# Kernel optimization log

Hardware: AMD Instinct MI355X
Metric: run time of the kernel (lower is better)

Reference implementation:

```python
import jax, jax.numpy as jnp
import numpy as np

E = 512      # moe_experts
M = 6        # per-expert dim = moe_dim // 2
H = 6        # moe_heads
D = 1024     # hidden_size
F = E * M    # flatten_shape = 3072

def relu2(x):
    return jnp.square(jax.nn.relu(x))

def setup_inputs() -> dict:
    key = jax.random.key(0)
    ks = jax.random.split(key, 12)
    B, S = 4, 2048
    inp = {
        "x": jax.random.normal(ks[0], (B, S, D), jnp.float32),
        "g1": jax.random.uniform(ks[1], (B, S, H, E), jnp.float32),
        "g2": jax.random.uniform(ks[2], (B, S, H, E), jnp.float32),
        "u1_w": jax.random.normal(ks[3], (F, D), jnp.float32) * 0.02,
        "u1_b": jnp.zeros((F,), jnp.float32),
        "u2_w": jax.random.normal(ks[4], (F, D), jnp.float32) * 0.02,
        "u2_b": jnp.zeros((F,), jnp.float32),
        "v11_w": jax.random.normal(ks[5], (D // 2, F), jnp.float32) * 0.02,
        "v12_w": jax.random.normal(ks[6], (D // 2, F), jnp.float32) * 0.02,
        "v21_w": jax.random.normal(ks[7], (D // 2, F), jnp.float32) * 0.02,
        "v22_w": jax.random.normal(ks[8], (D // 2, F), jnp.float32) * 0.02,
        "b1": jnp.zeros((E, D // 2), jnp.float32),
        "b2": jnp.zeros((E, D // 2), jnp.float32),
    }
    return inp

def reference(x, g1, g2, u1_w, u1_b, u2_w, u2_b, v11_w, v12_w, v21_w, v22_w, b1, b2):
    B, S, _ = x.shape
    # up-proj + relu^2, split into (experts E, per-expert dim M)
    x1 = relu2(x @ u1_w.T + u1_b).reshape(B, S, E, M)   # [B,S,E,M]
    x2 = relu2(x @ u2_w.T + u2_b).reshape(B, S, E, M)
    # gate sums over heads
    gs1 = jnp.einsum('bshi,bsim->bsim', g1, x1)          # sum_h g1 applied to x1
    gs2 = jnp.einsum('bshj,bsjm->bsjm', g2, x2)
    x11 = gs1.reshape(B, S, F) @ v11_w.T                 # [B,S,D/2]
    x22 = gs2.reshape(B, S, F) @ v22_w.T
    # cross terms: contract over h efficiently (avoid E x E materialization)
    t2 = jnp.einsum('bshj,bsjm->bshm', g2, x2)           # [B,S,H,M]
    x12 = jnp.einsum('bshm,bshi->bsim', t2, g1).reshape(B, S, F) @ v12_w.T
    t1 = jnp.einsum('bshi,bsim->bshm', g1, x1)
    x21 = jnp.einsum('bshm,bshj->bsjm', t1, g2).reshape(B, S, F) @ v21_w.T
    # bias terms through gates
    x13 = jnp.einsum('bshi,id->bsd', g1, b1)
    x23 = jnp.einsum('bshj,jd->bsd', g2, b2)
    return jnp.concatenate((x11 + x12 + x13, x21 + x22 + x23), axis=-1)
```

## Files before the change

### kernel.cpp

```cpp
#include <hip/hip_runtime.h>
#include <stdint.h>

typedef unsigned short u16;
typedef unsigned int u32;
typedef __attribute__((ext_vector_type(8))) short bf16x8;
typedef __attribute__((ext_vector_type(4))) float f32x4;

__device__ __forceinline__ float bf2f(u16 u) {
    unsigned v = ((unsigned)u) << 16;
    float f;
    __builtin_memcpy(&f, &v, 4);
    return f;
}
__device__ __forceinline__ u16 f2bf(float f) {
    unsigned x;
    __builtin_memcpy(&x, &f, 4);
    unsigned r = (x + 0x7fffu + ((x >> 16) & 1u)) >> 16;
    return (u16)r;
}

#define GLDS(g, l) __builtin_amdgcn_global_load_lds( \
    (const __attribute__((address_space(1))) void*)(g), \
    (__attribute__((address_space(3))) void*)(l), 16, 0, 0)

#define BARX() do { asm volatile("" ::: "memory"); __builtin_amdgcn_s_barrier(); asm volatile("" ::: "memory"); } while (0)
#define LGKM0() asm volatile("s_waitcnt lgkmcnt(0)" ::: "memory")
#define WAIT_VM4() asm volatile("s_waitcnt vmcnt(4)" ::: "memory")
#define WAIT_VM0() asm volatile("s_waitcnt vmcnt(0)" ::: "memory")

__device__ __forceinline__ void gemm256_core(
    const u16* gA, const u16* gB, size_t ldk, int NT,
    u16* lds, int tid, f32x4 (&acc)[8][4])
{
    const int lane  = tid & 63;
    const int wave  = tid >> 6;
    const int wr    = wave >> 2;
    const int wc    = wave & 3;
    const int mlane = lane & 15;
    const int quad  = lane >> 4;
    const int swz   = mlane & 7;

    u16* A0 = lds;
    u16* B0 = lds + 16384;
    u16* A1 = lds + 32768;
    u16* B1 = lds + 49152;

    #define ST_A(h, t, dst) do { \
        GLDS(gA + (size_t)((h)*128     ) * ldk + (size_t)(t) * 64, (dst) + (h)*8192 + tid*8); \
        GLDS(gA + (size_t)((h)*128 + 64) * ldk + (size_t)(t) * 64, (dst) + (h)*8192 + 4096 + tid*8); \
    } while (0)
    #define ST_B(h, t, dst) do { \
        GLDS(gB + (size_t)((h)*128     ) * ldk + (size_t)(t) * 64, (dst) + (h)*8192 + tid*8); \
        GLDS(gB + (size_t)((h)*128 + 64) * ldk + (size_t)(t) * 64, (dst) + (h)*8192 + 4096 + tid*8); \
    } while (0)
    #define RDA(mh) \
        _Pragma("unroll") \
        for (int m = 0; m < 4; ++m) { \
            const int rA = wr*128 + ((mh)*4 + m)*16 + mlane; \
            a[m][0] = *(const bf16x8*)(bA + rA*64 + (((0 + quad) ^ swz) * 8)); \
            a[m][1] = *(const bf16x8*)(bA + rA*64 + (((4 + quad) ^ swz) * 8)); \
        }
    #define RDB(nh) \
        _Pragma("unroll") \
        for (int n = 0; n < 2; ++n) { \
            const int rB = wc*64 + ((nh)*2 + n)*16 + mlane; \
            b[(nh)*2 + n][0] = *(const bf16x8*)(bB + rB*64 + (((0 + quad) ^ swz) * 8)); \
            b[(nh)*2 + n][1] = *(const bf16x8*)(bB + rB*64 + (((4 + quad) ^ swz) * 8)); \
        }
    #define MFMA_QUAD(MB, NB) do { \
        __builtin_amdgcn_s_setprio(1); \
        _Pragma("unroll") \
        for (int m = 0; m < 4; ++m) \
            _Pragma("unroll") \
            for (int n = 0; n < 2; ++n) \
                _Pragma("unroll") \
                for (int k = 0; k < 2; ++k) \
                    acc[(MB) + m][(NB) + n] = __builtin_amdgcn_mfma_f32_16x16x32_bf16( \
                        a[m][k], b[(NB) + n][k], acc[(MB) + m][(NB) + n], 0, 0, 0); \
        __builtin_amdgcn_s_setprio(0); \
    } while (0)

    ST_A(0, 0, A0); ST_A(1, 0, A0);
    ST_B(0, 0, B0); ST_B(1, 0, B0);
    ST_B(0, 1, B1); ST_B(1, 1, B1);
    WAIT_VM4();
    BARX();

    bf16x8 a[4][2], b[4][2];

    for (int u = 0; u < NT; ++u) {
        u16* bA = (u & 1) ? A1 : A0;
        u16* bB = (u & 1) ? B1 : B0;
        u16* oA = (u & 1) ? A0 : A1;

        RDA(0);
        RDB(0);
        if (u + 1 < NT) ST_A(0, u + 1, oA);
        BARX(); LGKM0();
        MFMA_QUAD(0, 0);
        BARX();

        RDB(1);
        if (u + 1 < NT) ST_A(1, u + 1, oA);
        BARX(); LGKM0();
        MFMA_QUAD(0, 2);
        BARX();

        RDA(1);
        if (u + 2 < NT) ST_B(0, u + 2, bB);
        BARX(); LGKM0();
        MFMA_QUAD(4, 2);
        BARX();

        if (u + 2 < NT) ST_B(1, u + 2, bB);
        BARX(); LGKM0();
        MFMA_QUAD(4, 0);
        if (u + 2 < NT) { WAIT_VM4(); } else { WAIT_VM0(); }
        BARX();
    }
    #undef ST_A
    #undef ST_B
    #undef RDA
    #undef RDB
    #undef MFMA_QUAD
}

__global__ __launch_bounds__(512, 2) void gemm1_8ph(
    const u16* __restrict__ X, const u16* __restrict__ U1, const u16* __restrict__ U2,
    const float* __restrict__ bias1, const float* __restrict__ bias2,
    u16* __restrict__ Y1, u16* __restrict__ Y2)
{
    __shared__ __align__(16) u16 lds[65536];
    const int tid = threadIdx.x;
    const int z = blockIdx.z;
    const int rowBase = blockIdx.y * 256;
    const int colBase = blockIdx.x * 256;
    const int r0 = tid >> 3;
    const int cs = ((tid & 7) ^ (r0 & 7)) * 8;
    const u16* gA = X + (size_t)(rowBase + r0) * 1024 + cs;
    const u16* gB = (z ? U2 : U1) + (size_t)(colBase + r0) * 1024 + cs;

    f32x4 acc[8][4] = {};
    gemm256_core(gA, gB, 1024, 16, lds, tid, acc);

    const float* bias = z ? bias2 : bias1;
    u16* outp = z ? Y2 : Y1;
    const int coloff = z * 3072;
    const int lane = tid & 63, wave = tid >> 6;
    const int wr = wave >> 2, wc = wave & 3;
    const int mlane = lane & 15, quad = lane >> 4;
    #pragma unroll
    for (int n = 0; n < 4; ++n) {
        const int col = colBase + wc * 64 + n * 16 + mlane;
        const float bv = bias[col];
        #pragma unroll
        for (int m = 0; m < 8; ++m) {
            const int rb = rowBase + wr * 128 + m * 16 + quad * 4;
            #pragma unroll
            for (int r = 0; r < 4; ++r) {
                float v = acc[m][n][r] + bv;
                v = (v > 0.0f) ? v * v : 0.0f;
                outp[(size_t)(rb + r) * 6656 + coloff + col] = f2bf(v);
            }
        }
    }
}

__global__ __launch_bounds__(512, 2) void gemm2_8ph(
    const u16* __restrict__ Y1, const u16* __restrict__ Y2,
    const u16* __restrict__ W1, const u16* __restrict__ W2,
    float* __restrict__ out, float* __restrict__ part, int nsplit)
{
    __shared__ __align__(16) u16 lds[65536];
    const int tid = threadIdx.x;
    const int z2 = blockIdx.z;
    const int z = z2 & 1;
    const int split = z2 >> 1;
    const int Ks = 6656 / nsplit;
    const int kbeg = split * Ks;
    const int rowBase = blockIdx.y * 256;
    const int colBase = blockIdx.x * 256;
    const int r0 = tid >> 3;
    const int cs = ((tid & 7) ^ (r0 & 7)) * 8;
    const u16* gA = (z ? Y2 : Y1) + (size_t)(rowBase + r0) * 6656 + kbeg + cs;
    const u16* gB = (z ? W2 : W1) + (size_t)(colBase + r0) * 6656 + kbeg + cs;

    f32x4 acc[8][4] = {};
    gemm256_core(gA, gB, 6656, Ks >> 6, lds, tid, acc);

    float* dst = split ? part : out;
    const int coloff = z * 512;
    const int lane = tid & 63, wave = tid >> 6;
    const int wr = wave >> 2, wc = wave & 3;
    const int mlane = lane & 15, quad = lane >> 4;
    #pragma unroll
    for (int n = 0; n < 4; ++n) {
        const int col = colBase + wc * 64 + n * 16 + mlane;
        #pragma unroll
        for (int m = 0; m < 8; ++m) {
            const int rb = rowBase + wr * 128 + m * 16 + quad * 4;
            #pragma unroll
            for (int r = 0; r < 4; ++r)
                dst[(size_t)(rb + r) * 1024 + coloff + col] = acc[m][n][r];
        }
    }
}

__global__ __launch_bounds__(256) void reduce_add(
    float4* __restrict__ out, const float4* __restrict__ p, int nadd)
{
    const int i = blockIdx.x * 256 + threadIdx.x;
    float4 v = out[i];
    for (int k = 0; k < nadd; ++k) {
        const float4 a = p[(size_t)k * 2097152 + i];
        v.x += a.x; v.y += a.y; v.z += a.z; v.w += a.w;
    }
    out[i] = v;
}

__global__ __launch_bounds__(256) void cvt_bf16(
    const float* __restrict__ x, const float* __restrict__ u1,
    const float* __restrict__ u2, u16* __restrict__ dst)
{
    const int idx4 = blockIdx.x * 256 + threadIdx.x;
    const int NX = 8388608 / 4, NU = 3145728 / 4;
    const float4* src;
    int off;
    if (idx4 < NX)           { src = (const float4*)x;  off = idx4; }
    else if (idx4 < NX + NU) { src = (const float4*)u1; off = idx4 - NX; }
    else                     { src = (const float4*)u2; off = idx4 - NX - NU; }
    const float4 v = src[off];
    ushort4 o;
    o.x = f2bf(v.x); o.y = f2bf(v.y); o.z = f2bf(v.z); o.w = f2bf(v.w);
    ((ushort4*)dst)[idx4] = o;
}

__global__ __launch_bounds__(256) void prep_wcat(
    const float* __restrict__ v11, const float* __restrict__ v12,
    const float* __restrict__ v21, const float* __restrict__ v22,
    const float* __restrict__ b1,  const float* __restrict__ b2,
    u16* __restrict__ W1, u16* __restrict__ W2)
{
    const int idx = blockIdx.x * 256 + threadIdx.x;
    const int n = idx / 6656;
    const int k = idx - n * 6656;
    float w1, w2;
    if (k < 3072)      { w1 = v11[n * 3072 + k];        w2 = v21[n * 3072 + k]; }
    else if (k < 6144) { w1 = v12[n * 3072 + k - 3072]; w2 = v22[n * 3072 + k - 3072]; }
    else               { w1 = b1[(k - 6144) * 512 + n]; w2 = b2[(k - 6144) * 512 + n]; }
    W1[idx] = f2bf(w1);
    W2[idx] = f2bf(w2);
}

__global__ __launch_bounds__(256) void gating(
    const float* __restrict__ g1, const float* __restrict__ g2,
    u16* __restrict__ Y1, u16* __restrict__ Y2)
{
    __shared__ __align__(16) u16 sm[17408];
    __shared__ float tls[72];
    u16* g1b = sm;
    u16* xT1 = sm + 3072;
    u16* g2b = sm + 6144;
    u16* xT2 = sm + 9216;
    const int tid = threadIdx.x;
    const int wave = tid >> 6, lane = tid & 63;
    const size_t tok = blockIdx.x;
    const size_t gb = tok * 3072;
    const size_t yb = tok * 6656;

    #pragma unroll
    for (int j = 0; j < 3; ++j) {
        const int c = tid + j * 256;
        float4 a = ((const float4*)(g1 + gb))[c];
        float4 bq = ((const float4*)(g2 + gb))[c];
        ushort4 oa, ob;
        oa.x = f2bf(a.x); oa.y = f2bf(a.y); oa.z = f2bf(a.z); oa.w = f2bf(a.w);
        ob.x = f2bf(bq.x); ob.y = f2bf(bq.y); ob.z = f2bf(bq.z); ob.w = f2bf(bq.w);
        ((ushort4*)g1b)[c] = oa;
        ((ushort4*)g2b)[c] = ob;
        ushort4 xv1 = ((const ushort4*)(Y1 + yb))[c];
        ushort4 xv2 = ((const ushort4*)(Y2 + yb + 3072))[c];
        const u16 v1[4] = {xv1.x, xv1.y, xv1.z, xv1.w};
        const u16 v2[4] = {xv2.x, xv2.y, xv2.z, xv2.w};
        #pragma unroll
        for (int q = 0; q < 4; ++q) {
            const int e = c * 4 + q;
            const int i = e / 6;
            const int m = e - 6 * i;
            xT1[m * 512 + i] = v1[q];
            xT2[m * 512 + i] = v2[q];
        }
    }
    __syncthreads();

    if (wave < 2) {
        const u16* Ab = wave ? g2b : g1b;
        const u16* Bb = wave ? xT2 : xT1;
        const int fofs = (lane & 15) * 512 + (lane >> 4) * 8;
        f32x4 acc = {};
        #pragma unroll
        for (int k0 = 0; k0 < 512; k0 += 32) {
            bf16x8 af = *(const bf16x8*)(Ab + fofs + k0);
            bf16x8 bf = *(const bf16x8*)(Bb + fofs + k0);
            acc = __builtin_amdgcn_mfma_f32_16x16x32_bf16(af, bf, acc, 0, 0, 0);
        }
        const int col = lane & 15;
        const int rowb = (lane >> 4) * 4;
        float* ts = tls + wave * 36;
        #pragma unroll
        for (int r = 0; r < 4; ++r) {
            const int row = rowb + r;
            if (row < 6 && col < 6) ts[row * 6 + col] = acc[r];
        }
    }
    __syncthreads();

    const int t = tid;
    u32* Y1d = (u32*)(Y1 + yb);
    u32* Y2d = (u32*)(Y2 + yb);
    float sp1[2], sp2[2];
    #pragma unroll
    for (int e = 0; e < 2; ++e) {
        const int i = 2 * t + e;
        float g1v[6], g2v[6];
        float s1 = 0.f, s2 = 0.f;
        #pragma unroll
        for (int h = 0; h < 6; ++h) {
            g1v[h] = bf2f(g1b[h * 512 + i]); s1 += g1v[h];
            g2v[h] = bf2f(g2b[h * 512 + i]); s2 += g2v[h];
        }
        sp1[e] = s1; sp2[e] = s2;
        u32 pa1[3], pc2[3], pc1[3], pa2[3];
        #pragma unroll
        for (int mq = 0; mq < 3; ++mq) {
            u32 wa1 = 0, wc2 = 0, wc1 = 0, wa2 = 0;
            #pragma unroll
            for (int half = 0; half < 2; ++half) {
                const int m = mq * 2 + half;
                const float x1 = bf2f(xT1[m * 512 + i]);
                const float x2 = bf2f(xT2[m * 512 + i]);
                const float a1 = s1 * x1;
                const float a2 = s2 * x2;
                float c1 = 0.f, c2 = 0.f;
                #pragma unroll
                for (int h = 0; h < 6; ++h) {
                    c2 += tls[36 + h * 6 + m] * g1v[h];
                    c1 += tls[h * 6 + m] * g2v[h];
                }
                const int sh = half * 16;
                wa1 |= ((u32)f2bf(a1)) << sh;
                wc2 |= ((u32)f2bf(c2)) << sh;
                wc1 |= ((u32)f2bf(c1)) << sh;
                wa2 |= ((u32)f2bf(a2)) << sh;
            }
            pa1[mq] = wa1; pc2[mq] = wc2; pc1[mq] = wc1; pa2[mq] = wa2;
        }
        const int base = 6 * t + 3 * e;
        #pragma unroll
        for (int mq = 0; mq < 3; ++mq) {
            Y1d[base + mq]        = pa1[mq];
            Y1d[1536 + base + mq] = pc2[mq];
            Y2d[base + mq]        = pc1[mq];
            Y2d[1536 + base + mq] = pa2[mq];
        }
    }
    Y1d[3072 + t] = (u32)f2bf(sp1[0]) | (((u32)f2bf(sp1[1])) << 16);
    Y2d[3072 + t] = (u32)f2bf(sp2[0]) | (((u32)f2bf(sp2[1])) << 16);
}

extern "C" void kernel_launch(void* const* d_in, const int* in_sizes, int n_in,
                              void* d_out, int out_size, void* d_ws, size_t ws_size,
                              hipStream_t stream) {
    const float* x   = (const float*)d_in[0];
    const float* g1  = (const float*)d_in[1];
    const float* g2  = (const float*)d_in[2];
    const float* u1w = (const float*)d_in[3];
    const float* u1b = (const float*)d_in[4];
    const float* u2w = (const float*)d_in[5];
    const float* u2b = (const float*)d_in[6];
    const float* v11 = (const float*)d_in[7];
    const float* v12 = (const float*)d_in[8];
    const float* v21 = (const float*)d_in[9];
    const float* v22 = (const float*)d_in[10];
    const float* b1  = (const float*)d_in[11];
    const float* b2  = (const float*)d_in[12];
    float* out = (float*)d_out;

    u16* Y1   = (u16*)d_ws;
    u16* Y2   = Y1 + (size_t)8192 * 6656;
    u16* xbf  = Y2 + (size_t)8192 * 6656;
    u16* u1bf = xbf + (size_t)8192 * 1024;
    u16* u2bf = u1bf + (size_t)3072 * 1024;
    u16* W1   = u2bf + (size_t)3072 * 1024;
    u16* W2   = W1 + (size_t)512 * 6656;
    float* part = (float*)(W2 + (size_t)512 * 6656);

    const size_t base = (size_t)(W2 + (size_t)512 * 6656 - (u16*)d_ws) * 2;
    const size_t pbytes = (size_t)8192 * 1024 * 4;
    const int nsplit = (ws_size >= base + pbytes) ? 2 : 1;

    cvt_bf16<<<dim3(14336), 256, 0, stream>>>(x, u1w, u2w, xbf);
    prep_wcat<<<dim3(13312), 256, 0, stream>>>(v11, v12, v21, v22, b1, b2, W1, W2);

    gemm1_8ph<<<dim3(12, 32, 2), 512, 0, stream>>>(
        xbf, u1bf, u2bf, u1b, u2b, Y1, Y2);

    gating<<<dim3(8192), 256, 0, stream>>>(g1, g2, Y1, Y2);

    gemm2_8ph<<<dim3(2, 32, 2 * nsplit), 512, 0, stream>>>(
        Y1, Y2, W1, W2, out, part, nsplit);
    if (nsplit > 1)
        reduce_add<<<dim3(8192), 256, 0, stream>>>(
            (float4*)out, (const float4*)part, nsplit - 1);
}
```

Baseline: 586.2 us.

## Software-pipeline LDS fragment reads against MFMAs and drop most per-iteration barriers

Restructures the bf16 GEMM main loop so that A/B fragments are read from LDS one K-half at a time into separate register sets. Those reads are interleaved with the MFMA groups that consume the previously loaded fragments. The first fragments of the next tile are prefetched after the end-of-iteration barrier. The number of workgroup barriers per K-tile drops from eight to two, and global-to-LDS stores are regrouped around them. The aim is to hide LDS latency behind matrix math and cut synchronization stalls, at the cost of tighter ordering assumptions on buffer reuse and possibly different register pressure.

```diff
diff --git a/kernel.cpp b/kernel.cpp
--- a/kernel.cpp
+++ b/kernel.cpp
@@ -53,30 +53,28 @@
         GLDS(gB + (size_t)((h)*128     ) * ldk + (size_t)(t) * 64, (dst) + (h)*8192 + tid*8); \
         GLDS(gB + (size_t)((h)*128 + 64) * ldk + (size_t)(t) * 64, (dst) + (h)*8192 + 4096 + tid*8); \
     } while (0)
-    #define RDA(mh) \
+    #define RD_A(dst, buf, mh, kh) do { \
         _Pragma("unroll") \
         for (int m = 0; m < 4; ++m) { \
-            const int rA = wr*128 + ((mh)*4 + m)*16 + mlane; \
-            a[m][0] = *(const bf16x8*)(bA + rA*64 + (((0 + quad) ^ swz) * 8)); \
-            a[m][1] = *(const bf16x8*)(bA + rA*64 + (((4 + quad) ^ swz) * 8)); \
-        }
-    #define RDB(nh) \
+            const int r = wr*128 + ((mh)*4 + m)*16 + mlane; \
+            dst[m] = *(const bf16x8*)((buf) + r*64 + ((((kh)*4 + quad) ^ swz) * 8)); \
+        } \
+    } while (0)
+    #define RD_B(dst, buf, nh, kh) do { \
         _Pragma("unroll") \
         for (int n = 0; n < 2; ++n) { \
-            const int rB = wc*64 + ((nh)*2 + n)*16 + mlane; \
-            b[(nh)*2 + n][0] = *(const bf16x8*)(bB + rB*64 + (((0 + quad) ^ swz) * 8)); \
-            b[(nh)*2 + n][1] = *(const bf16x8*)(bB + rB*64 + (((4 + quad) ^ swz) * 8)); \
-        }
-    #define MFMA_QUAD(MB, NB) do { \
+            const int r = wc*64 + ((nh)*2 + n)*16 + mlane; \
+            dst[n] = *(const bf16x8*)((buf) + r*64 + ((((kh)*4 + quad) ^ swz) * 8)); \
+        } \
+    } while (0)
+    #define MM8(aS, bS, MB, NB) do { \
         __builtin_amdgcn_s_setprio(1); \
         _Pragma("unroll") \
         for (int m = 0; m < 4; ++m) \
             _Pragma("unroll") \
             for (int n = 0; n < 2; ++n) \
-                _Pragma("unroll") \
-                for (int k = 0; k < 2; ++k) \
-                    acc[(MB) + m][(NB) + n] = __builtin_amdgcn_mfma_f32_16x16x32_bf16( \
-                        a[m][k], b[(NB) + n][k], acc[(MB) + m][(NB) + n], 0, 0, 0); \
+                acc[(MB) + m][(NB) + n] = __builtin_amdgcn_mfma_f32_16x16x32_bf16( \
+                    aS[m], bS[n], acc[(MB) + m][(NB) + n], 0, 0, 0); \
         __builtin_amdgcn_s_setprio(0); \
     } while (0)
 
@@ -86,43 +84,48 @@
     WAIT_VM4();
     BARX();
 
-    bf16x8 a[4][2], b[4][2];
+    bf16x8 a0[4], a1[4], b0[2], b1[2];
+    RD_A(a0, A0, 0, 0);
+    RD_B(b0, B0, 0, 0);
 
     for (int u = 0; u < NT; ++u) {
         u16* bA = (u & 1) ? A1 : A0;
         u16* bB = (u & 1) ? B1 : B0;
         u16* oA = (u & 1) ? A0 : A1;
-
-        RDA(0);
-        RDB(0);
-        if (u + 1 < NT) ST_A(0, u + 1, oA);
-        BARX(); LGKM0();
-        MFMA_QUAD(0, 0);
+        u16* nB = (u & 1) ? B0 : B1;
+
+        RD_A(a1, bA, 1, 0);
+        MM8(a0, b0, 0, 0);
+        RD_B(b1, bB, 1, 0);
+        MM8(a1, b0, 4, 0);
+        MM8(a1, b1, 4, 2);
+        RD_A(a1, bA, 0, 1);
+        RD_B(b0, bB, 1, 1);
+        MM8(a0, b1, 0, 2);
+        RD_A(a0, bA, 1, 1);
+        if (u + 1 < NT) { ST_A(0, u + 1, oA); ST_A(1, u + 1, oA); }
+        MM8(a1, b0, 0, 2);
+        RD_B(b1, bB, 0, 1);
+        MM8(a0, b0, 4, 2);
+        LGKM0();
         BARX();
-
-        RDB(1);
-        if (u + 1 < NT) ST_A(1, u + 1, oA);
-        BARX(); LGKM0();
-        MFMA_QUAD(0, 2);
-        BARX();
-
-        RDA(1);
         if (u + 2 < NT) ST_B(0, u + 2, bB);
-        BARX(); LGKM0();
-        MFMA_QUAD(4, 2);
-        BARX();
-
+        MM8(a0, b1, 4, 0);
         if (u + 2 < NT) ST_B(1, u + 2, bB);
-        BARX(); LGKM0();
-        MFMA_QUAD(4, 0);
-        if (u + 2 < NT) { WAIT_VM4(); } else { WAIT_VM0(); }
-        BARX();
+        MM8(a1, b1, 0, 0);
+
+        if (u + 1 < NT) {
+            if (u + 2 < NT) { WAIT_VM4(); } else { WAIT_VM0(); }
+            BARX();
+            RD_A(a0, oA, 0, 0);
+            RD_B(b0, nB, 0, 0);
+        }
     }
     #undef ST_A
     #undef ST_B
-    #undef RDA
-    #undef RDB
-    #undef MFMA_QUAD
+    #undef RD_A
+    #undef RD_B
+    #undef MM8
 }
 
 __global__ __launch_bounds__(512, 2) void gemm1_8ph(
```

Measured after the change: 586.0 us. About the same (-0.0%).
